# Kernel optimization log

Hardware: AMD Instinct MI355X
Metric: run time of the kernel (lower is better)

## Reference

```python
import jax, jax.numpy as jnp
import numpy as np

N = 100000      # total nodes (10 graphs x 10000)
E = 1600000     # edges, avg degree 16
HN = 64         # hidden_node_dim
HE = 16         # hidden_edge_dim
IN_N, IN_E = 3, 1
L = 3           # conv_layers
B = 10          # num_graphs
NEG_SLOPE = 0.2
BN_EPS = 1e-5


def setup_inputs() -> dict:
    key = jax.random.key(0)
    ks = jax.random.split(key, 8)
    s = lambda d: 1.0 / np.sqrt(d)
    return {
        "x": jax.random.normal(ks[0], (N, IN_N), jnp.float32),
        "edge_attr": jax.random.uniform(ks[1], (E, IN_E), jnp.float32),
        "edge_index": jax.random.randint(ks[2], (2, E), 0, N, jnp.int64),
        "fc_node_w": jax.random.normal(ks[3], (IN_N, HN), jnp.float32) * s(IN_N),
        "fc_node_b": jnp.zeros((HN,), jnp.float32),
        "fc_edge_w": jax.random.normal(ks[4], (IN_E, HE), jnp.float32) * s(IN_E),
        "fc_edge_b": jnp.zeros((HE,), jnp.float32),
        "bn_gamma": jnp.ones((HN,), jnp.float32),
        "bn_beta": jnp.zeros((HN,), jnp.float32),
        "fc_w": jax.random.normal(ks[5], (L, HN, HN), jnp.float32) * s(HN),
        "fc_b": jnp.zeros((L, HN), jnp.float32),
        "attn_w": jax.random.normal(ks[6], (L, 2 * HN + HE, HN), jnp.float32) * s(2 * HN + HE),
        "attn_b": jnp.zeros((L, HN), jnp.float32),
        "batch_size": B,
    }


def segment_softmax(alpha, idx, num_segments):
    # PyG softmax: per-target-node, per-channel, numerically stable
    amax = jax.ops.segment_max(alpha, idx, num_segments=num_segments)
    amax = jnp.where(jnp.isfinite(amax), amax, 0.0)  # empty segments -> -inf
    ex = jnp.exp(alpha - amax[idx])
    denom = jax.ops.segment_sum(ex, idx, num_segments=num_segments)
    return ex / (denom[idx] + 1e-16)


def reference(x, edge_attr, edge_index, fc_node_w, fc_node_b, fc_edge_w, fc_edge_b,
              bn_gamma, bn_beta, fc_w, fc_b, attn_w, attn_b, batch_size):
    h = x @ fc_node_w + fc_node_b                 # [N, HN]
    e = edge_attr @ fc_edge_w + fc_edge_b        # [E, HE]
    # BatchNorm1d (training-mode batch statistics, biased variance)
    mean = jnp.mean(h, axis=0)
    var = jnp.mean((h - mean) ** 2, axis=0)
    h = (h - mean) * jax.lax.rsqrt(var + BN_EPS) * bn_gamma + bn_beta

    src, dst = edge_index[0], edge_index[1]      # x_j = h[src], x_i = h[dst]
    for l in range(L):
        hl = h @ fc_w[l] + fc_b[l]               # [N, HN]
        xi = hl[dst]                             # [E, HN]
        xj = hl[src]                             # [E, HN]
        cat = jnp.concatenate([xi, xj, e], axis=-1)  # [E, 2*HN+HE]
        alpha = cat @ attn_w[l] + attn_b[l]      # [E, HN]
        alpha = jax.nn.leaky_relu(alpha, NEG_SLOPE)
        alpha = segment_softmax(alpha, dst, N)
        h = jax.ops.segment_sum(xj * alpha, dst, num_segments=N)  # scatter-add aggregate
    return h.reshape(batch_size, -1, HN)
```

## Files before the change

kernel.cpp:

```cpp
#include <hip/hip_runtime.h>
#include <math.h>

#define NN 100000
#define NE 1600000
#define LAYERS 3
#define NEG 0.2f
#define BN_EPS 1e-5f

#define NB 196
#define NWG 512
#define CHUNK 3125
#define MOMB 304
#define TFB 1563

typedef __attribute__((ext_vector_type(8))) short bf16x8;
typedef __attribute__((ext_vector_type(4))) float f32x4;

__device__ __forceinline__ unsigned f2bf(float x) {
    unsigned u = __float_as_uint(x);
    return (u + 0x7fffu + ((u >> 16) & 1u)) >> 16;
}

__global__ __launch_bounds__(256) void k_front(const int* __restrict__ ei,
    int* __restrict__ counts, const float* __restrict__ x, float* __restrict__ mom)
{
    int t = threadIdx.x;
    if (blockIdx.x < NWG) {
        __shared__ int hist[NB];
        int wg = blockIdx.x;
        if (t < NB) hist[t] = 0;
        __syncthreads();
        int base = wg * CHUNK;
        for (int i = t; i < CHUNK; i += 256)
            atomicAdd(&hist[ei[NE + base + i] >> 9], 1);
        __syncthreads();
        if (t < NB) counts[wg * NB + t] = hist[t];
    } else {
        int mb = blockIdx.x - NWG;
        float s0=0,s1=0,s2=0,m00=0,m01=0,m02=0,m11=0,m12=0,m22=0;
        for (int n = mb * 256 + t; n < NN; n += MOMB * 256) {
            float a = x[n*3], b = x[n*3+1], c = x[n*3+2];
            s0 += a; s1 += b; s2 += c;
            m00 = fmaf(a,a,m00); m01 = fmaf(a,b,m01); m02 = fmaf(a,c,m02);
            m11 = fmaf(b,b,m11); m12 = fmaf(b,c,m12); m22 = fmaf(c,c,m22);
        }
        #pragma unroll
        for (int off = 32; off; off >>= 1) {
            s0 += __shfl_xor(s0, off); s1 += __shfl_xor(s1, off); s2 += __shfl_xor(s2, off);
            m00 += __shfl_xor(m00, off); m01 += __shfl_xor(m01, off); m02 += __shfl_xor(m02, off);
            m11 += __shfl_xor(m11, off); m12 += __shfl_xor(m12, off); m22 += __shfl_xor(m22, off);
        }
        __shared__ float red[4][9];
        int wave = t >> 6, lane = t & 63;
        if (lane == 0) {
            red[wave][0]=s0; red[wave][1]=s1; red[wave][2]=s2;
            red[wave][3]=m00; red[wave][4]=m01; red[wave][5]=m02;
            red[wave][6]=m11; red[wave][7]=m12; red[wave][8]=m22;
        }
        __syncthreads();
        if (t < 9) {
            float v = red[0][t] + red[1][t] + red[2][t] + red[3][t];
            atomicAdd(&mom[t], v);
        }
    }
}

__device__ __forceinline__ float bn_scale_of(const float* __restrict__ mom,
    const float* __restrict__ fnw, const float* __restrict__ fnb,
    const float* __restrict__ gamma, int k)
{
    float w0 = fnw[k], w1 = fnw[64 + k], w2 = fnw[128 + k], bc = fnb[k];
    float dot  = mom[0]*w0 + mom[1]*w1 + mom[2]*w2;
    float quad = mom[3]*w0*w0 + 2.f*mom[4]*w0*w1 + 2.f*mom[5]*w0*w2
               + mom[6]*w1*w1 + 2.f*mom[7]*w1*w2 + mom[8]*w2*w2;
    float mean = dot * (1.0f / NN) + bc;
    float eh2  = quad * (1.0f / NN) + 2.f * bc * dot * (1.0f / NN) + bc * bc;
    float var  = eh2 - mean * mean;
    return gamma[k] * rsqrtf(var + BN_EPS);
}

__global__ __launch_bounds__(256) void k_mid(const float* __restrict__ mom,
    const float* __restrict__ fnw, const float* __restrict__ fnb,
    const float* __restrict__ gamma, const float* __restrict__ beta,
    const float* __restrict__ few, const float* __restrict__ feb,
    const float* __restrict__ attn_w, const float* __restrict__ attn_b,
    const float* __restrict__ fcb, const float* __restrict__ fcw,
    int* __restrict__ counts, int* __restrict__ bbase, int* __restrict__ row_ptr,
    float* __restrict__ u, float* __restrict__ c0, float* __restrict__ feff,
    unsigned short* __restrict__ wt)
{
    int t = threadIdx.x;
    if (blockIdx.x == 0) {
        __shared__ float ssh[64], sfe[3][64];
        if (t < 64) {
            float w0 = fnw[t], w1 = fnw[64 + t], w2 = fnw[128 + t], bc = fnb[t];
            float dot  = mom[0]*w0 + mom[1]*w1 + mom[2]*w2;
            float quad = mom[3]*w0*w0 + 2.f*mom[4]*w0*w1 + 2.f*mom[5]*w0*w2
                       + mom[6]*w1*w1 + 2.f*mom[7]*w1*w2 + mom[8]*w2*w2;
            float mean = dot * (1.0f / NN) + bc;
            float eh2  = quad * (1.0f / NN) + 2.f * bc * dot * (1.0f / NN) + bc * bc;
            float var  = eh2 - mean * mean;
            float sc   = gamma[t] * rsqrtf(var + BN_EPS);
            ssh[t] = beta[t] - mean * sc;
        }
        __syncthreads();
        if (t < 64) {
            float v = 0.f;
            for (int k = 0; k < 64; k++) v = fmaf(ssh[k], fcw[k * 64 + t], v);
            sfe[0][t] = fcb[t] + v;
            sfe[1][t] = fcb[64 + t];
            sfe[2][t] = fcb[128 + t];
        }
        __syncthreads();
        if (t < 192) {
            int l = t >> 6, c = t & 63;
            const float* AW = attn_w + l * 144 * 64;
            float uu = 0.f, cc = 0.f;
            for (int j = 0; j < 16; j++) {
                float wv = AW[(128 + j) * 64 + c];
                uu = fmaf(few[j], wv, uu);
                cc = fmaf(feb[j], wv, cc);
            }
            float bi = 0.f;
            for (int tt = 0; tt < 64; tt++)
                bi = fmaf(sfe[l][tt], AW[tt * 64 + c] + AW[(64 + tt) * 64 + c], bi);
            u[t]    = uu;
            c0[t]   = cc + attn_b[t] + bi;
            feff[t] = sfe[l][c];
        }
    } else if (blockIdx.x == 1) {
        __shared__ int s_tot[256];
        int tot = 0;
        if (t < NB)
            for (int w = 0; w < NWG; w++) tot += counts[w * NB + t];
        s_tot[t] = tot;
        __syncthreads();
        for (int off = 1; off < 256; off <<= 1) {
            int v = (t >= off) ? s_tot[t - off] : 0;
            __syncthreads();
            s_tot[t] += v;
            __syncthreads();
        }
        int excl = s_tot[t] - tot;
        if (t < NB) {
            bbase[t] = excl;
            int run = excl;
            for (int w = 0; w < NWG; w++) {
                int c = counts[w * NB + t];
                counts[w * NB + t] = run;
                run += c;
            }
            if (t == NB - 1) {
                bbase[NB] = run;
                row_ptr[NN] = run;
            }
        }
    } else {
        int task = (blockIdx.x - 2) * 4 + (t >> 6);
        int k = t & 63;
        int l = task / 192, g = task - l * 192;
        const float* W0 = fcw + l * 4096;
        float scale = (l == 0) ? bn_scale_of(mom, fnw, fnb, gamma, k) : 1.0f;
        float v;
        if (g < 64) {
            v = W0[k * 64 + g] * scale;
        } else {
            int c = g & 63;
            const float* Wx = attn_w + l * 144 * 64 + (g < 128 ? 0 : 4096);
            float s = 0.f;
            for (int tt = 0; tt < 64; tt++) s = fmaf(W0[k * 64 + tt], Wx[tt * 64 + c], s);
            v = s * scale;
        }
        wt[(l * 192 + g) * 64 + k] = (unsigned short)f2bf(v);
    }
}

__device__ __forceinline__ void tf_core(const bf16x8* a, const unsigned short* __restrict__ wt_l,
    const float* __restrict__ feff_l, const float* __restrict__ c0_l,
    float* __restrict__ ai, unsigned* __restrict__ packed, int n0, int r16, int quad)
{
    f32x4 acc[12];
    #pragma unroll
    for (int i = 0; i < 12; i++) acc[i] = (f32x4){0.f, 0.f, 0.f, 0.f};
    const unsigned short* wb = wt_l + (size_t)r16 * 64 + quad * 8;
    #pragma unroll
    for (int cb = 0; cb < 12; cb++) {
        bf16x8 b0 = *(const bf16x8*)(wb + cb * 1024);
        bf16x8 b1 = *(const bf16x8*)(wb + cb * 1024 + 32);
        acc[cb] = __builtin_amdgcn_mfma_f32_16x16x32_bf16(a[0], b0, acc[cb], 0, 0, 0);
        acc[cb] = __builtin_amdgcn_mfma_f32_16x16x32_bf16(a[1], b1, acc[cb], 0, 0, 0);
    }
    #pragma unroll
    for (int r = 0; r < 4; r++) {
        int nd = n0 + quad * 4 + r;
        if (nd < NN) {
            size_t base = (size_t)nd * 64 + r16;
            #pragma unroll
            for (int cq = 0; cq < 4; cq++) {
                float hlv = acc[cq][r] + feff_l[cq * 16 + r16];
                float aiv = acc[4 + cq][r] + c0_l[cq * 16 + r16];
                float ajv = acc[8 + cq][r];
                ai[base + cq * 16]     = aiv;
                packed[base + cq * 16] = f2bf(hlv) | (f2bf(ajv) << 16);
            }
        }
    }
}

__global__ __launch_bounds__(256) void k_l3(const int* __restrict__ ei,
    const float* __restrict__ ea, const int* __restrict__ counts, int2* __restrict__ brec,
    const float* __restrict__ xin, const float* __restrict__ fnw, const float* __restrict__ fnb,
    const unsigned short* __restrict__ wt, const float* __restrict__ feff,
    const float* __restrict__ c0v, float* __restrict__ ai, unsigned* __restrict__ packed)
{
    int t = threadIdx.x;
    if (blockIdx.x < NWG) {
        __shared__ int off[NB];
        int wg = blockIdx.x;
        if (t < NB) off[t] = counts[wg * NB + t];
        __syncthreads();
        int base = wg * CHUNK;
        for (int i = t; i < CHUNK; i += 256) {
            int k = base + i;
            int s = ei[k], d = ei[NE + k];
            int b = d >> 9;
            int j = atomicAdd(&off[b], 1);
            brec[j] = make_int2(((d & 511) << 17) | s, __float_as_int(ea[k]));
        }
    } else {
        int bid = blockIdx.x - NWG;
        int wv = t >> 6, l = t & 63;
        int r16 = l & 15, quad = l >> 4;
        int n0 = bid * 64 + wv * 16;
        int na = n0 + r16; if (na >= NN) na = NN - 1;
        float x0 = xin[na*3], x1 = xin[na*3+1], x2 = xin[na*3+2];
        bf16x8 a[2];
        #pragma unroll
        for (int ks = 0; ks < 2; ks++) {
            bf16x8 tt;
            #pragma unroll
            for (int e = 0; e < 8; e++) {
                int c = quad * 8 + ks * 32 + e;
                float v = fmaf(x0, fnw[c], fmaf(x1, fnw[64 + c], fmaf(x2, fnw[128 + c], fnb[c])));
                tt[e] = (short)f2bf(v);
            }
            a[ks] = tt;
        }
        tf_core(a, wt, feff, c0v, ai, packed, n0, r16, quad);
    }
}

__global__ __launch_bounds__(256) void k_csr(const int2* __restrict__ brec,
    const int* __restrict__ bbase, int* __restrict__ row_ptr, int2* __restrict__ er)
{
    __shared__ int s_cnt[512], s_excl[512], s_ts[256];
    int t = threadIdx.x, b = blockIdx.x;
    int beg = bbase[b], end = bbase[b + 1];
    s_cnt[t] = 0; s_cnt[t + 256] = 0;
    __syncthreads();
    for (int i = beg + t; i < end; i += 256)
        atomicAdd(&s_cnt[brec[i].x >> 17], 1);
    __syncthreads();
    int a0 = s_cnt[2 * t], a1 = s_cnt[2 * t + 1];
    int ts = a0 + a1;
    s_ts[t] = ts;
    __syncthreads();
    for (int off = 1; off < 256; off <<= 1) {
        int v = (t >= off) ? s_ts[t - off] : 0;
        __syncthreads();
        s_ts[t] += v;
        __syncthreads();
    }
    int et = s_ts[t] - ts;
    s_excl[2 * t] = et; s_excl[2 * t + 1] = et + a0;
    s_cnt[t] = 0; s_cnt[t + 256] = 0;
    __syncthreads();
    #pragma unroll
    for (int q = 0; q < 2; q++) {
        int dl = t + q * 256;
        int n = b * 512 + dl;
        if (n < NN) row_ptr[n] = beg + s_excl[dl];
    }
    for (int i = beg + t; i < end; i += 256) {
        int2 r = brec[i];
        int dl = r.x >> 17;
        int pos = atomicAdd(&s_cnt[dl], 1);
        er[beg + s_excl[dl] + pos] = make_int2(r.x & 0x1FFFF, r.y);
    }
}

__global__ __launch_bounds__(256) void k_tf(const float* __restrict__ h,
    const unsigned short* __restrict__ wt_l, const float* __restrict__ feff_l,
    const float* __restrict__ c0_l, float* __restrict__ ai, unsigned* __restrict__ packed)
{
    int t = threadIdx.x;
    int wv = t >> 6, l = t & 63;
    int r16 = l & 15, quad = l >> 4;
    int n0 = blockIdx.x * 64 + wv * 16;
    int na = n0 + r16; if (na >= NN) na = NN - 1;
    const float* hp = h + (size_t)na * 64 + quad * 8;
    bf16x8 a[2];
    #pragma unroll
    for (int ks = 0; ks < 2; ks++) {
        f32x4 lo = *(const f32x4*)(hp + ks * 32);
        f32x4 hi = *(const f32x4*)(hp + ks * 32 + 4);
        bf16x8 tt;
        tt[0] = (short)f2bf(lo[0]); tt[1] = (short)f2bf(lo[1]);
        tt[2] = (short)f2bf(lo[2]); tt[3] = (short)f2bf(lo[3]);
        tt[4] = (short)f2bf(hi[0]); tt[5] = (short)f2bf(hi[1]);
        tt[6] = (short)f2bf(hi[2]); tt[7] = (short)f2bf(hi[3]);
        a[ks] = tt;
    }
    tf_core(a, wt_l, feff_l, c0_l, ai, packed, n0, r16, quad);
}

__global__ __launch_bounds__(256) void k_edge(const unsigned* __restrict__ packed,
    const float* __restrict__ ai, const int* __restrict__ row_ptr,
    const int2* __restrict__ er, const float* __restrict__ u_l,
    float* __restrict__ hout)
{
    int w = threadIdx.x >> 6, c = threadIdx.x & 63;
    int n = blockIdx.x * 4 + w;
    int beg = row_ptr[n], end = row_ptr[n + 1];
    float base = ai[n * 64 + c];
    float uc = u_l[c];
    const unsigned* __restrict__ pc = packed + c;
    float d0 = 0.f, d1 = 0.f, s0 = 0.f, s1 = 0.f;
    int k = beg;
    for (; k + 16 <= end; k += 16) {
        int2 e[16]; unsigned p[16];
        #pragma unroll
        for (int q = 0; q < 16; q++) e[q] = er[k + q];
        #pragma unroll
        for (int q = 0; q < 16; q++) p[q] = pc[(size_t)e[q].x << 6];
        #pragma unroll
        for (int q = 0; q < 16; q++) {
            float a = fmaf(__int_as_float(e[q].y), uc, base + __uint_as_float(p[q] & 0xffff0000u));
            a = fmaxf(a, NEG * a);
            float xx = __expf(a);
            if (q & 1) { d1 += xx; s1 = fmaf(xx, __uint_as_float(p[q] << 16), s1); }
            else       { d0 += xx; s0 = fmaf(xx, __uint_as_float(p[q] << 16), s0); }
        }
    }
    for (; k + 8 <= end; k += 8) {
        int2 e[8]; unsigned p[8];
        #pragma unroll
        for (int q = 0; q < 8; q++) e[q] = er[k + q];
        #pragma unroll
        for (int q = 0; q < 8; q++) p[q] = pc[(size_t)e[q].x << 6];
        #pragma unroll
        for (int q = 0; q < 8; q++) {
            float a = fmaf(__int_as_float(e[q].y), uc, base + __uint_as_float(p[q] & 0xffff0000u));
            a = fmaxf(a, NEG * a);
            float xx = __expf(a);
            if (q & 1) { d1 += xx; s1 = fmaf(xx, __uint_as_float(p[q] << 16), s1); }
            else       { d0 += xx; s0 = fmaf(xx, __uint_as_float(p[q] << 16), s0); }
        }
    }
    for (; k + 4 <= end; k += 4) {
        int2 e[4]; unsigned p[4];
        #pragma unroll
        for (int q = 0; q < 4; q++) e[q] = er[k + q];
        #pragma unroll
        for (int q = 0; q < 4; q++) p[q] = pc[(size_t)e[q].x << 6];
        #pragma unroll
        for (int q = 0; q < 4; q++) {
            float a = fmaf(__int_as_float(e[q].y), uc, base + __uint_as_float(p[q] & 0xffff0000u));
            a = fmaxf(a, NEG * a);
            float xx = __expf(a);
            if (q & 1) { d1 += xx; s1 = fmaf(xx, __uint_as_float(p[q] << 16), s1); }
            else       { d0 += xx; s0 = fmaf(xx, __uint_as_float(p[q] << 16), s0); }
        }
    }
    for (; k < end; k++) {
        int2 e0 = er[k];
        unsigned p0 = pc[(size_t)e0.x << 6];
        float a0 = fmaf(__int_as_float(e0.y), uc, base + __uint_as_float(p0 & 0xffff0000u));
        a0 = fmaxf(a0, NEG * a0);
        float x0 = __expf(a0);
        d0 += x0;
        s0 = fmaf(x0, __uint_as_float(p0 << 16), s0);
    }
    hout[n * 64 + c] = (s0 + s1) / (d0 + d1 + 1e-16f);
}

extern "C" void kernel_launch(void* const* d_in, const int* in_sizes, int n_in,
                              void* d_out, int out_size, void* d_ws, size_t ws_size,
                              hipStream_t stream)
{
    const float* x    = (const float*)d_in[0];
    const float* ea   = (const float*)d_in[1];
    const int*   ei   = (const int*)d_in[2];
    const float* fnw  = (const float*)d_in[3];
    const float* fnb  = (const float*)d_in[4];
    const float* few  = (const float*)d_in[5];
    const float* feb  = (const float*)d_in[6];
    const float* gmm  = (const float*)d_in[7];
    const float* beta = (const float*)d_in[8];
    const float* fcw  = (const float*)d_in[9];
    const float* fcb  = (const float*)d_in[10];
    const float* aw   = (const float*)d_in[11];
    const float* ab   = (const float*)d_in[12];
    float* out = (float*)d_out;

    char* ws = (char*)d_ws;
    size_t off = 0;
    auto alloc = [&](size_t bytes) -> void* {
        void* p = ws + off;
        off += (bytes + 255) / 256 * 256;
        return p;
    };
    float*    h       = (float*)   alloc((size_t)NN * 64 * 4);
    float*    ai      = (float*)   alloc((size_t)NN * 64 * 4);
    unsigned* packed  = (unsigned*)alloc((size_t)NN * 64 * 4);
    int2*     er      = (int2*)    alloc((size_t)NE * 8);
    int2*     brec    = (int2*)    alloc((size_t)NE * 8);
    int*      row_ptr = (int*)     alloc((size_t)(NN + 1) * 4);
    int*      counts  = (int*)     alloc((size_t)NB * NWG * 4);
    int*      bbase   = (int*)     alloc((NB + 1) * 4);
    float*    mom     = (float*)   alloc(12 * 4);
    float*    uvec    = (float*)   alloc(192 * 4);
    float*    c0vec   = (float*)   alloc(192 * 4);
    float*    feff    = (float*)   alloc(192 * 4);
    unsigned short* wt = (unsigned short*)alloc((size_t)LAYERS * 192 * 64 * 2);

    (void)hipMemsetAsync(mom, 0, 12 * 4, stream);

    k_front<<<NWG + MOMB, 256, 0, stream>>>(ei, counts, x, mom);
    k_mid<<<2 + 144, 256, 0, stream>>>(mom, fnw, fnb, gmm, beta, few, feb, aw, ab,
                                       fcb, fcw, counts, bbase, row_ptr,
                                       uvec, c0vec, feff, wt);
    k_l3<<<NWG + TFB, 256, 0, stream>>>(ei, ea, counts, brec, x, fnw, fnb,
                                        wt, feff, c0vec, ai, packed);
    k_csr<<<NB, 256, 0, stream>>>(brec, bbase, row_ptr, er);
    k_edge<<<NN / 4, 256, 0, stream>>>(packed, ai, row_ptr, er, uvec, h);
    k_tf<<<TFB, 256, 0, stream>>>(h, wt + (size_t)192 * 64, feff + 64, c0vec + 64, ai, packed);
    k_edge<<<NN / 4, 256, 0, stream>>>(packed, ai, row_ptr, er, uvec + 64, h);
    k_tf<<<TFB, 256, 0, stream>>>(h, wt + (size_t)2 * 192 * 64, feff + 128, c0vec + 128, ai, packed);
    k_edge<<<NN / 4, 256, 0, stream>>>(packed, ai, row_ptr, er, uvec + 128, out);
    (void)in_sizes; (void)n_in; (void)out_size; (void)ws_size;
}
```

Before: 441.9 us.

## Fuse edge aggregation with next-layer MFMA transform and fold log2e into weights

Merges the per-layer edge softmax/aggregation kernel with the following layer's bf16 MFMA node transform. Each wave now aggregates 16 nodes in sequence, stages their results in LDS and feeds them straight to tf_core, so the fp32 h buffer is never written to or re-read from global memory. The packed buffer is double-buffered so one layer reads while the next writes. Separately, log2(e) is folded into the attention weights and biases so the inner loop can use a native exp2 instead of expf. The trade-off is fewer waves, each doing sequential per-node work, which weakens latency hiding and can worsen load imbalance across nodes of different degree.

```diff
diff --git a/kernel.cpp b/kernel.cpp
--- a/kernel.cpp
+++ b/kernel.cpp
@@ -6,6 +6,7 @@
 #define LAYERS 3
 #define NEG 0.2f
 #define BN_EPS 1e-5f
+#define LOG2E 1.4426950408889634f
 
 #define NB 196
 #define NWG 512
@@ -15,6 +16,12 @@
 
 typedef __attribute__((ext_vector_type(8))) short bf16x8;
 typedef __attribute__((ext_vector_type(4))) float f32x4;
+
+#if __has_builtin(__builtin_amdgcn_exp2f)
+#define EXP2(x) __builtin_amdgcn_exp2f(x)
+#else
+#define EXP2(x) __expf((x) * 0.6931471805599453f)
+#endif
 
 __device__ __forceinline__ unsigned f2bf(float x) {
     unsigned u = __float_as_uint(x);
@@ -124,8 +131,8 @@
             float bi = 0.f;
             for (int tt = 0; tt < 64; tt++)
                 bi = fmaf(sfe[l][tt], AW[tt * 64 + c] + AW[(64 + tt) * 64 + c], bi);
-            u[t]    = uu;
-            c0[t]   = cc + attn_b[t] + bi;
+            u[t]    = uu * LOG2E;
+            c0[t]   = (cc + attn_b[t] + bi) * LOG2E;
             feff[t] = sfe[l][c];
         }
     } else if (blockIdx.x == 1) {
@@ -169,7 +176,7 @@
             const float* Wx = attn_w + l * 144 * 64 + (g < 128 ? 0 : 4096);
             float s = 0.f;
             for (int tt = 0; tt < 64; tt++) s = fmaf(W0[k * 64 + tt], Wx[tt * 64 + c], s);
-            v = s * scale;
+            v = s * scale * LOG2E;
         }
         wt[(l * 192 + g) * 64 + k] = (unsigned short)f2bf(v);
     }
@@ -289,99 +296,93 @@
     }
 }
 
-__global__ __launch_bounds__(256) void k_tf(const float* __restrict__ h,
-    const unsigned short* __restrict__ wt_l, const float* __restrict__ feff_l,
-    const float* __restrict__ c0_l, float* __restrict__ ai, unsigned* __restrict__ packed)
-{
+#define EDGE_STEP(q, dacc, sacc) { \
+    float aa = fmaf(__int_as_float(e[q].y), uc, base + __uint_as_float(p[q] & 0xffff0000u)); \
+    aa = fmaxf(aa, NEG * aa); \
+    float xx = EXP2(aa); \
+    dacc += xx; sacc = fmaf(xx, __uint_as_float(p[q] << 16), sacc); }
+
+template<int DOTF>
+__global__ __launch_bounds__(256) void k_edgetf(const unsigned* __restrict__ packed_r,
+    float* __restrict__ ai, const int* __restrict__ row_ptr,
+    const int2* __restrict__ er, const float* __restrict__ u_l,
+    const unsigned short* __restrict__ wt_n, const float* __restrict__ feff_n,
+    const float* __restrict__ c0_n, unsigned* __restrict__ packed_w,
+    float* __restrict__ outp)
+{
+    __shared__ float hlds[64][68];
     int t = threadIdx.x;
-    int wv = t >> 6, l = t & 63;
-    int r16 = l & 15, quad = l >> 4;
-    int n0 = blockIdx.x * 64 + wv * 16;
-    int na = n0 + r16; if (na >= NN) na = NN - 1;
-    const float* hp = h + (size_t)na * 64 + quad * 8;
-    bf16x8 a[2];
-    #pragma unroll
-    for (int ks = 0; ks < 2; ks++) {
-        f32x4 lo = *(const f32x4*)(hp + ks * 32);
-        f32x4 hi = *(const f32x4*)(hp + ks * 32 + 4);
-        bf16x8 tt;
-        tt[0] = (short)f2bf(lo[0]); tt[1] = (short)f2bf(lo[1]);
-        tt[2] = (short)f2bf(lo[2]); tt[3] = (short)f2bf(lo[3]);
-        tt[4] = (short)f2bf(hi[0]); tt[5] = (short)f2bf(hi[1]);
-        tt[6] = (short)f2bf(hi[2]); tt[7] = (short)f2bf(hi[3]);
-        a[ks] = tt;
-    }
-    tf_core(a, wt_l, feff_l, c0_l, ai, packed, n0, r16, quad);
-}
-
-__global__ __launch_bounds__(256) void k_edge(const unsigned* __restrict__ packed,
-    const float* __restrict__ ai, const int* __restrict__ row_ptr,
-    const int2* __restrict__ er, const float* __restrict__ u_l,
-    float* __restrict__ hout)
-{
-    int w = threadIdx.x >> 6, c = threadIdx.x & 63;
-    int n = blockIdx.x * 4 + w;
-    int beg = row_ptr[n], end = row_ptr[n + 1];
-    float base = ai[n * 64 + c];
-    float uc = u_l[c];
-    const unsigned* __restrict__ pc = packed + c;
-    float d0 = 0.f, d1 = 0.f, s0 = 0.f, s1 = 0.f;
-    int k = beg;
-    for (; k + 16 <= end; k += 16) {
-        int2 e[16]; unsigned p[16];
+    int wv = t >> 6, lane = t & 63;
+    int nbase = blockIdx.x * 64 + wv * 16;
+    float uc = u_l[lane];
+    const unsigned* __restrict__ pc = packed_r + lane;
+    for (int m = 0; m < 16; m++) {
+        int n = nbase + m;
+        if (n >= NN) break;
+        int beg = row_ptr[n], end = row_ptr[n + 1];
+        float base = ai[(size_t)n * 64 + lane];
+        float d0 = 0.f, d1 = 0.f, s0 = 0.f, s1 = 0.f;
+        int k = beg;
+        for (; k + 16 <= end; k += 16) {
+            int2 e[16]; unsigned p[16];
+            #pragma unroll
+            for (int q = 0; q < 16; q++) e[q] = er[k + q];
+            #pragma unroll
+            for (int q = 0; q < 16; q++) p[q] = pc[(size_t)e[q].x << 6];
+            #pragma unroll
+            for (int q = 0; q < 16; q++) {
+                if (q & 1) EDGE_STEP(q, d1, s1) else EDGE_STEP(q, d0, s0)
+            }
+        }
+        for (; k + 8 <= end; k += 8) {
+            int2 e[8]; unsigned p[8];
+            #pragma unroll
+            for (int q = 0; q < 8; q++) e[q] = er[k + q];
+            #pragma unroll
+            for (int q = 0; q < 8; q++) p[q] = pc[(size_t)e[q].x << 6];
+            #pragma unroll
+            for (int q = 0; q < 8; q++) {
+                if (q & 1) EDGE_STEP(q, d1, s1) else EDGE_STEP(q, d0, s0)
+            }
+        }
+        for (; k + 4 <= end; k += 4) {
+            int2 e[4]; unsigned p[4];
+            #pragma unroll
+            for (int q = 0; q < 4; q++) e[q] = er[k + q];
+            #pragma unroll
+            for (int q = 0; q < 4; q++) p[q] = pc[(size_t)e[q].x << 6];
+            #pragma unroll
+            for (int q = 0; q < 4; q++) {
+                if (q & 1) EDGE_STEP(q, d1, s1) else EDGE_STEP(q, d0, s0)
+            }
+        }
+        for (; k < end; k++) {
+            int2 e[1]; unsigned p[1];
+            e[0] = er[k];
+            p[0] = pc[(size_t)e[0].x << 6];
+            EDGE_STEP(0, d0, s0)
+        }
+        float hv = (s0 + s1) / (d0 + d1 + 1e-16f);
+        if (DOTF) hlds[wv * 16 + m][lane] = hv;
+        else      outp[(size_t)n * 64 + lane] = hv;
+    }
+    if (DOTF) {
+        int r16 = lane & 15, quad = lane >> 4;
+        const float* hp = &hlds[wv * 16 + r16][quad * 8];
+        bf16x8 a[2];
         #pragma unroll
-        for (int q = 0; q < 16; q++) e[q] = er[k + q];
-        #pragma unroll
-        for (int q = 0; q < 16; q++) p[q] = pc[(size_t)e[q].x << 6];
-        #pragma unroll
-        for (int q = 0; q < 16; q++) {
-            float a = fmaf(__int_as_float(e[q].y), uc, base + __uint_as_float(p[q] & 0xffff0000u));
-            a = fmaxf(a, NEG * a);
-            float xx = __expf(a);
-            if (q & 1) { d1 += xx; s1 = fmaf(xx, __uint_as_float(p[q] << 16), s1); }
-            else       { d0 += xx; s0 = fmaf(xx, __uint_as_float(p[q] << 16), s0); }
-        }
-    }
-    for (; k + 8 <= end; k += 8) {
-        int2 e[8]; unsigned p[8];
-        #pragma unroll
-        for (int q = 0; q < 8; q++) e[q] = er[k + q];
-        #pragma unroll
-        for (int q = 0; q < 8; q++) p[q] = pc[(size_t)e[q].x << 6];
-        #pragma unroll
-        for (int q = 0; q < 8; q++) {
-            float a = fmaf(__int_as_float(e[q].y), uc, base + __uint_as_float(p[q] & 0xffff0000u));
-            a = fmaxf(a, NEG * a);
-            float xx = __expf(a);
-            if (q & 1) { d1 += xx; s1 = fmaf(xx, __uint_as_float(p[q] << 16), s1); }
-            else       { d0 += xx; s0 = fmaf(xx, __uint_as_float(p[q] << 16), s0); }
-        }
-    }
-    for (; k + 4 <= end; k += 4) {
-        int2 e[4]; unsigned p[4];
-        #pragma unroll
-        for (int q = 0; q < 4; q++) e[q] = er[k + q];
-        #pragma unroll
-        for (int q = 0; q < 4; q++) p[q] = pc[(size_t)e[q].x << 6];
-        #pragma unroll
-        for (int q = 0; q < 4; q++) {
-            float a = fmaf(__int_as_float(e[q].y), uc, base + __uint_as_float(p[q] & 0xffff0000u));
-            a = fmaxf(a, NEG * a);
-            float xx = __expf(a);
-            if (q & 1) { d1 += xx; s1 = fmaf(xx, __uint_as_float(p[q] << 16), s1); }
-            else       { d0 += xx; s0 = fmaf(xx, __uint_as_float(p[q] << 16), s0); }
-        }
-    }
-    for (; k < end; k++) {
-        int2 e0 = er[k];
-        unsigned p0 = pc[(size_t)e0.x << 6];
-        float a0 = fmaf(__int_as_float(e0.y), uc, base + __uint_as_float(p0 & 0xffff0000u));
-        a0 = fmaxf(a0, NEG * a0);
-        float x0 = __expf(a0);
-        d0 += x0;
-        s0 = fmaf(x0, __uint_as_float(p0 << 16), s0);
-    }
-    hout[n * 64 + c] = (s0 + s1) / (d0 + d1 + 1e-16f);
+        for (int ks = 0; ks < 2; ks++) {
+            f32x4 lo = *(const f32x4*)(hp + ks * 32);
+            f32x4 hi = *(const f32x4*)(hp + ks * 32 + 4);
+            bf16x8 tt;
+            tt[0] = (short)f2bf(lo[0]); tt[1] = (short)f2bf(lo[1]);
+            tt[2] = (short)f2bf(lo[2]); tt[3] = (short)f2bf(lo[3]);
+            tt[4] = (short)f2bf(hi[0]); tt[5] = (short)f2bf(hi[1]);
+            tt[6] = (short)f2bf(hi[2]); tt[7] = (short)f2bf(hi[3]);
+            a[ks] = tt;
+        }
+        tf_core(a, wt_n, feff_n, c0_n, ai, packed_w, nbase, r16, quad);
+    }
 }
 
 extern "C" void kernel_launch(void* const* d_in, const int* in_sizes, int n_in,
@@ -410,9 +411,9 @@
         off += (bytes + 255) / 256 * 256;
         return p;
     };
-    float*    h       = (float*)   alloc((size_t)NN * 64 * 4);
     float*    ai      = (float*)   alloc((size_t)NN * 64 * 4);
-    unsigned* packed  = (unsigned*)alloc((size_t)NN * 64 * 4);
+    unsigned* packed0 = (unsigned*)alloc((size_t)NN * 64 * 4);
+    unsigned* packed1 = (unsigned*)alloc((size_t)NN * 64 * 4);
     int2*     er      = (int2*)    alloc((size_t)NE * 8);
     int2*     brec    = (int2*)    alloc((size_t)NE * 8);
     int*      row_ptr = (int*)     alloc((size_t)(NN + 1) * 4);
@@ -431,12 +432,15 @@
                                        fcb, fcw, counts, bbase, row_ptr,
                                        uvec, c0vec, feff, wt);
     k_l3<<<NWG + TFB, 256, 0, stream>>>(ei, ea, counts, brec, x, fnw, fnb,
-                                        wt, feff, c0vec, ai, packed);
+                                        wt, feff, c0vec, ai, packed0);
     k_csr<<<NB, 256, 0, stream>>>(brec, bbase, row_ptr, er);
-    k_edge<<<NN / 4, 256, 0, stream>>>(packed, ai, row_ptr, er, uvec, h);
-    k_tf<<<TFB, 256, 0, stream>>>(h, wt + (size_t)192 * 64, feff + 64, c0vec + 64, ai, packed);
-    k_edge<<<NN / 4, 256, 0, stream>>>(packed, ai, row_ptr, er, uvec + 64, h);
-    k_tf<<<TFB, 256, 0, stream>>>(h, wt + (size_t)2 * 192 * 64, feff + 128, c0vec + 128, ai, packed);
-    k_edge<<<NN / 4, 256, 0, stream>>>(packed, ai, row_ptr, er, uvec + 128, out);
+    k_edgetf<1><<<TFB, 256, 0, stream>>>(packed0, ai, row_ptr, er, uvec,
+                                         wt + (size_t)192 * 64, feff + 64, c0vec + 64,
+                                         packed1, out);
+    k_edgetf<1><<<TFB, 256, 0, stream>>>(packed1, ai, row_ptr, er, uvec + 64,
+                                         wt + (size_t)2 * 192 * 64, feff + 128, c0vec + 128,
+                                         packed0, out);
+    k_edgetf<0><<<TFB, 256, 0, stream>>>(packed0, ai, row_ptr, er, uvec + 128,
+                                         wt, feff, c0vec, packed1, out);
     (void)in_sizes; (void)n_in; (void)out_size; (void)ws_size;
 }
```

Result: slower. 497.1 us (+12.5%).
